# Kernel optimization log

Hardware: AMD Instinct MI355X
Metric: run time of the kernel (lower is better)

The kernel has to match this reference:

```python
import jax, jax.numpy as jnp
import numpy as np

# Constants from UpFIRDn2dJIT(channel=64, lrelu_upsampling=2, filter_size=6, kernel_size=3)
# with init_kernel(in_size=128, out_size=128): up_factor = dn_factor = 2.
UP = 2
DN = 2
SLOPE = 0.2
GAIN = 1.4142135623730951  # sqrt(2)
CROP = 1  # kernel_size - 1 - kernel_size//2 for kernel_size=3
IN_SIZE = 128
FILTER_SIZE = 6
B, C = 8, 64


def _firwin_lowpass(numtaps, cutoff, width, fs):
    # Reproduces scipy.signal.firwin(numtaps, cutoff, width=width, fs=fs)
    # (lowpass, pass_zero=True, scale=True, Kaiser window from `width`).
    nyq = 0.5 * fs
    atten = 2.285 * (numtaps - 1) * np.pi * (width / nyq) + 7.95  # kaiser_atten
    if atten > 50:
        beta = 0.1102 * (atten - 8.7)
    elif atten > 21:
        beta = 0.5842 * (atten - 21) ** 0.4 + 0.07886 * (atten - 21)
    else:
        beta = 0.0
    m = np.arange(numtaps) - (numtaps - 1) / 2.0
    c = cutoff / nyq
    h = c * np.sinc(c * m) * np.kaiser(numtaps, beta)
    h = h / h.sum()  # scale so DC gain == 1
    return h.astype(np.float32)


def _conv1d_same(x, f, axis):
    # x: [N, 1, H, W]; 1D cross-correlation along `axis` (2 or 3) with torch
    # padding='same' semantics for even taps: left pad = (K-1)//2, right pad gets the extra.
    K = f.shape[0]
    pl = (K - 1) // 2
    pr = (K - 1) - pl
    if axis == 2:
        kern = f.reshape(1, 1, K, 1)
        pad = [(pl, pr), (0, 0)]
    else:
        kern = f.reshape(1, 1, 1, K)
        pad = [(0, 0), (pl, pr)]
    return jax.lax.conv_general_dilated(
        x, kern, window_strides=(1, 1), padding=pad,
        dimension_numbers=("NCHW", "OIHW", "NCHW"))


def _forward(x, bias, up_filter, dn_filter):
    x = x[:, :, CROP:-CROP, CROP:-CROP]            # [B, C, 128, 128]
    b, c, h, w = x.shape
    x = x + bias[None, :, None, None]
    x = x.reshape(b * c, 1, h, w)
    x = jnp.repeat(jnp.repeat(x, UP, axis=2), UP, axis=3)
    # outer(f, f) conv == separable 1D convs (filter is an outer product)
    x = _conv1d_same(_conv1d_same(x, up_filter, 2), up_filter, 3)
    x = jnp.where(x >= 0, x, SLOPE * x) * GAIN     # leaky ReLU * gain
    x = _conv1d_same(_conv1d_same(x, dn_filter, 2), dn_filter, 3)
    x = x[:, :, ::DN, ::DN]                        # grid_pool2d -> [B*C, 1, 128, 128]
    return x.reshape(b, c, x.shape[2], x.shape[3])


def setup_inputs() -> dict:
    key = jax.random.key(0)
    kx, = jax.random.split(key, 1)
    x = jax.random.normal(kx, (B, C, IN_SIZE + 2 * CROP, IN_SIZE + 2 * CROP), dtype=jnp.float32)
    bias = jnp.zeros((C,), dtype=jnp.float32)  # nn.Parameter init to zeros
    taps = FILTER_SIZE * UP  # 12
    up_filter = jnp.asarray(_firwin_lowpass(taps, IN_SIZE / 2.0001, IN_SIZE, IN_SIZE))
    dn_filter = jnp.asarray(_firwin_lowpass(taps, IN_SIZE / 2.0001, IN_SIZE, IN_SIZE))
    return {"x": x, "bias": bias, "up_filter": up_filter, "dn_filter": dn_filter}


def reference(x, bias, up_filter, dn_filter):
    return _forward(x, bias, up_filter, dn_filter)
```

## Files before the change

kernel.cpp:

```cpp
#include <hip/hip_runtime.h>


#define GAIN_C 1.4142135623730951f
#define NEG_C ((0.2f - 1.0f) * GAIN_C)

typedef short v8s __attribute__((ext_vector_type(8)));
typedef float v4f __attribute__((ext_vector_type(4)));

__device__ __forceinline__ int f2bf(float f) {
    unsigned u = __float_as_uint(f);
    return (int)((u + 0x7FFFu + ((u >> 16) & 1u)) >> 16) & 0xFFFF;
}
__device__ __forceinline__ int pack_bf2(float a, float b) {
#if __has_builtin(__builtin_amdgcn_cvt_pk_bf16_f32)
    typedef __bf16 bf2 __attribute__((ext_vector_type(2)));
    bf2 r = __builtin_amdgcn_cvt_pk_bf16_f32(a, b);
    int o; __builtin_memcpy(&o, &r, 4); return o;
#else
    return f2bf(a) | (f2bf(b) << 16);
#endif
}

__device__ float band(int x, int q, const float* fu) {
    if (q >= 74 || x >= 43 || x < 0) return 0.f;
    int p = q >> 1, d = x - p;
    if (q & 1) {
        if (d < 0 || d > 6) return 0.f;
        if (d == 0) return fu[0];
        if (d == 6) return fu[11];
        return fu[2 * d - 1] + fu[2 * d];
    } else {
        if (d < 0 || d > 5) return 0.f;
        return fu[2 * d] + fu[2 * d + 1];
    }
}
__device__ float dband(int o, int q, int v, const float* fd) {
    if (q >= 74 || q < 0) return 0.f;
    if (v == 0 && q < 5) return 0.f;
    if (v == 2 && q >= 69) return 0.f;
    int k = q - 2 * o;
    if (k < 0 || k > 11) return 0.f;
    return fd[k];
}

__global__ __launch_bounds__(256) void build_consts(
    const float* __restrict__ fu, const float* __restrict__ fd,
    short* __restrict__ ws)
{
    int idx = blockIdx.x * 256 + threadIdx.x;
    int l = (idx >> 3) & 63, j = idx & 7;
    int l15 = l & 15, kq = (l >> 4) * 8 + j;
    float val;
    if (idx < 2560) {
        int nt = idx >> 9;
        int k0 = 8 * nt < 16 ? 8 * nt : 16;
        val = band(k0 + kq, 16 * nt + l15, fu);
    } else if (idx < 5120) {
        int mt = (idx - 2560) >> 9;
        int k0 = 8 * mt < 16 ? 8 * mt : 16;
        val = band(k0 + kq, 16 * mt + l15, fu);
    } else if (idx < 11264) {
        int rel = idx - 5120;
        int v = rel >> 11, fi = (rel & 2047) >> 9;
        int mt = fi >> 1, kt = fi & 1;
        int pp = (mt ? 16 : 0) + 32 * kt + kq;
        val = dband(16 * mt + l15, pp, v, fd);
    } else {
        int rel = idx - 11264;
        int v = rel >> 11, fi = (rel & 2047) >> 9;
        int nt = fi >> 1, kt = fi & 1;
        int qq = (nt ? 16 : 0) + 32 * kt + kq;
        val = dband(16 * nt + l15, qq, v, fd);
    }
    ws[idx] = (short)f2bf(val);
}

#define XPITCH 48
#define BPITCH 48
#define UPITCH 88
#define TPITCH 80

__global__ __launch_bounds__(320, 8) void upfirdn_mfma(
    const float* __restrict__ xin_all,
    const float* __restrict__ bias,
    const short* __restrict__ cws,
    float* __restrict__ out)
{
    __shared__ __align__(16) short SH[2304 + 3840 + 7040];
    short* Xl  = SH;
    short* B1t = SH + 2304;
    short* Ut  = SH + 6144;
    short* T   = SH;

    const int tid  = threadIdx.x;
    const int lane = tid & 63, w = tid >> 6;
    const int l15  = lane & 15, q4 = lane >> 4;
    const int bx = blockIdx.x, by = blockIdx.y, bc = blockIdx.z;
    const int i0 = by * 32, j0 = bx * 32;

    const short* GtB = cws;
    const short* G2A = cws + 2560;
    const short* DA  = cws + 5120  + ((by == 0) ? 0 : (by == 3) ? 2 : 1) * 2048;
    const short* D2B = cws + 11264 + ((bx == 0) ? 0 : (bx == 3) ? 2 : 1) * 2048;

    {
        const float* xp = xin_all + (size_t)bc * (130 * 130);
        const float bv = bias[bc & 63];
        const bool colInt = (bx == 1) | (bx == 2);
        int* Xli = (int*)Xl;
        for (int idx = tid; idx < 1152; idx += 320) {
            int r = idx / 24, cp = idx - r * 24;
            int gr = i0 - 5 + r;
            float f0 = 0.f, f1 = 0.f;
            if (r < 43 && (unsigned)gr < 128u && cp < 22) {
                const float* rowp = xp + (gr + 1) * 130 + 1;
                int gc0 = j0 - 5 + 2 * cp;
                if (colInt) {
                    f0 = rowp[gc0] + bv;
                    if (cp < 21) f1 = rowp[gc0 + 1] + bv;
                } else {
                    if ((unsigned)gc0 < 128u) f0 = rowp[gc0] + bv;
                    if (cp < 21 && (unsigned)(gc0 + 1) < 128u)
                        f1 = rowp[gc0 + 1] + bv;
                }
            }
            Xli[r * 24 + cp] = pack_bf2(f0, f1);
        }
    }
    __syncthreads();

    {
        const int nt = w;
        const int k0 = 8 * nt < 16 ? 8 * nt : 16;
        v8s bf = *(const v8s*)&GtB[nt * 512 + lane * 8];
#pragma unroll
        for (int mt = 0; mt < 3; ++mt) {
            v8s a = *(const v8s*)&Xl[(16 * mt + l15) * XPITCH + k0 + q4 * 8];
            v4f acc = {0.f, 0.f, 0.f, 0.f};
            acc = __builtin_amdgcn_mfma_f32_16x16x32_bf16(a, bf, acc, 0, 0, 0);
            *(int2*)&B1t[(16 * nt + l15) * BPITCH + 16 * mt + q4 * 4] =
                make_int2(pack_bf2(acc[0], acc[1]), pack_bf2(acc[2], acc[3]));
        }
    }
    __syncthreads();

    {
        const int mt = w;
        const int k0 = 8 * mt < 16 ? 8 * mt : 16;
        v8s af = *(const v8s*)&G2A[mt * 512 + lane * 8];
#pragma unroll
        for (int nt = 0; nt < 5; ++nt) {
            v8s b = *(const v8s*)&B1t[(16 * nt + l15) * BPITCH + k0 + q4 * 8];
            v4f acc = {0.f, 0.f, 0.f, 0.f};
            acc = __builtin_amdgcn_mfma_f32_16x16x32_bf16(af, b, acc, 0, 0, 0);
#pragma unroll
            for (int i = 0; i < 4; ++i)
                acc[i] = GAIN_C * acc[i] + NEG_C * fminf(acc[i], 0.f);
            *(int2*)&Ut[(16 * nt + l15) * UPITCH + 16 * mt + q4 * 4] =
                make_int2(pack_bf2(acc[0], acc[1]), pack_bf2(acc[2], acc[3]));
        }
    }
    __syncthreads();

    {
        const int nt = w;
#pragma unroll
        for (int mt = 0; mt < 2; ++mt) {
            const int k0 = mt ? 16 : 0;
            v4f acc = {0.f, 0.f, 0.f, 0.f};
#pragma unroll
            for (int kt = 0; kt < 2; ++kt) {
                v8s a = *(const v8s*)&DA[(mt * 2 + kt) * 512 + lane * 8];
                v8s b = *(const v8s*)&Ut[(16 * nt + l15) * UPITCH
                                         + k0 + 32 * kt + q4 * 8];
                acc = __builtin_amdgcn_mfma_f32_16x16x32_bf16(a, b, acc, 0, 0, 0);
            }
#pragma unroll
            for (int i = 0; i < 4; ++i)
                T[(16 * mt + q4 * 4 + i) * TPITCH + 16 * nt + l15] =
                    (short)f2bf(acc[i]);
        }
    }
    __syncthreads();

    if (w < 4) {
        const int mt = w >> 1, nt = w & 1;
        const int k0 = nt ? 16 : 0;
        v4f acc = {0.f, 0.f, 0.f, 0.f};
#pragma unroll
        for (int kt = 0; kt < 2; ++kt) {
            v8s a = *(const v8s*)&T[(16 * mt + l15) * TPITCH + k0 + 32 * kt + q4 * 8];
            v8s b = *(const v8s*)&D2B[(nt * 2 + kt) * 512 + lane * 8];
            acc = __builtin_amdgcn_mfma_f32_16x16x32_bf16(a, b, acc, 0, 0, 0);
        }
        float* op = out + (size_t)bc * 16384
                  + (size_t)(i0 + 16 * mt + q4 * 4) * 128 + (j0 + 16 * nt + l15);
#pragma unroll
        for (int i = 0; i < 4; ++i) op[i * 128] = acc[i];
    }
}

extern "C" void kernel_launch(void* const* d_in, const int* in_sizes, int n_in,
                              void* d_out, int out_size, void* d_ws, size_t ws_size,
                              hipStream_t stream) {
    const float* x  = (const float*)d_in[0];
    const float* bs = (const float*)d_in[1];
    const float* fu = (const float*)d_in[2];
    const float* fd = (const float*)d_in[3];
    float* outp = (float*)d_out;
    short* ws = (short*)d_ws;

    build_consts<<<68, 256, 0, stream>>>(fu, fd, ws);
    upfirdn_mfma<<<dim3(4, 4, 512), 320, 0, stream>>>(x, bs, ws, outp);
}
```

Measured before the change: 124.1 us.

## Process two channel planes per block and reorder separable conv passes

Each block now handles two (batch, channel) planes, halving the grid, and loads the constant filter matrices into registers once per block for reuse across both planes. The column and row pass order is swapped, so the transposed scalar writes of the intermediate are replaced by packed int2 stores, and interior row tiles skip bounds checks and use float2 loads. This amortizes constant loads and sync overhead per plane, but doubles shared memory per block and lowers the occupancy hint from 8 to 4 blocks.

```diff
diff --git a/kernel.cpp b/kernel.cpp
--- a/kernel.cpp
+++ b/kernel.cpp
@@ -75,128 +75,142 @@
     ws[idx] = (short)f2bf(val);
 }
 
-#define XPITCH 48
-#define BPITCH 48
-#define UPITCH 88
-#define TPITCH 80
-
-__global__ __launch_bounds__(320, 8) void upfirdn_mfma(
+#define XP2 48
+#define BP2 48
+#define UP2 88
+#define RSZ 13184
+
+__global__ __launch_bounds__(320, 4) void upfirdn_mfma(
     const float* __restrict__ xin_all,
     const float* __restrict__ bias,
     const short* __restrict__ cws,
     float* __restrict__ out)
 {
-    __shared__ __align__(16) short SH[2304 + 3840 + 7040];
-    short* Xl  = SH;
-    short* B1t = SH + 2304;
-    short* Ut  = SH + 6144;
-    short* T   = SH;
+    __shared__ __align__(16) short SH[2 * RSZ];
 
     const int tid  = threadIdx.x;
     const int lane = tid & 63, w = tid >> 6;
     const int l15  = lane & 15, q4 = lane >> 4;
-    const int bx = blockIdx.x, by = blockIdx.y, bc = blockIdx.z;
+    const int bx = blockIdx.x, by = blockIdx.y;
+    const int bc0 = blockIdx.z * 2;
     const int i0 = by * 32, j0 = bx * 32;
 
-    const short* GtB = cws;
-    const short* G2A = cws + 2560;
-    const short* DA  = cws + 5120  + ((by == 0) ? 0 : (by == 3) ? 2 : 1) * 2048;
-    const short* D2B = cws + 11264 + ((bx == 0) ? 0 : (bx == 3) ? 2 : 1) * 2048;
+    const short* DAv  = cws + 5120  + ((by == 0) ? 0 : (by == 3) ? 2 : 1) * 2048;
+    const short* D2Bv = cws + 11264 + ((bx == 0) ? 0 : (bx == 3) ? 2 : 1) * 2048;
+    v8s gtb = *(const v8s*)&cws[w * 512 + lane * 8];
+    v8s g2a = *(const v8s*)&cws[2560 + w * 512 + lane * 8];
+    v8s d2b[4];
+#pragma unroll
+    for (int f = 0; f < 4; ++f) d2b[f] = *(const v8s*)&D2Bv[f * 512 + lane * 8];
+    const int mt4 = (w >> 1) & 1;
+    v8s da0 = *(const v8s*)&DAv[(mt4 * 2 + 0) * 512 + lane * 8];
+    v8s da1 = *(const v8s*)&DAv[(mt4 * 2 + 1) * 512 + lane * 8];
 
     {
-        const float* xp = xin_all + (size_t)bc * (130 * 130);
-        const float bv = bias[bc & 63];
+        const float* xp0 = xin_all + (size_t)bc0 * 16900;
+        const float* xp1 = xp0 + 16900;
+        const float bv0 = bias[bc0 & 63], bv1 = bias[(bc0 + 1) & 63];
+        const bool rowInt = (by == 1) | (by == 2);
         const bool colInt = (bx == 1) | (bx == 2);
-        int* Xli = (int*)Xl;
-        for (int idx = tid; idx < 1152; idx += 320) {
-            int r = idx / 24, cp = idx - r * 24;
+        int* Xli = (int*)SH;
+        for (int idx = tid; idx < 2304; idx += 320) {
+            int pl = (idx >= 1152);
+            int ii = idx - (pl ? 1152 : 0);
+            int r = ii / 24, cp = ii - r * 24;
             int gr = i0 - 5 + r;
+            const float* xp = pl ? xp1 : xp0;
+            const float bv = pl ? bv1 : bv0;
             float f0 = 0.f, f1 = 0.f;
-            if (r < 43 && (unsigned)gr < 128u && cp < 22) {
+            bool rok = (r < 43) && (rowInt || (unsigned)gr < 128u);
+            if (rok && cp < 22) {
+                int gc0 = j0 - 5 + 2 * cp;
                 const float* rowp = xp + (gr + 1) * 130 + 1;
-                int gc0 = j0 - 5 + 2 * cp;
                 if (colInt) {
-                    f0 = rowp[gc0] + bv;
-                    if (cp < 21) f1 = rowp[gc0 + 1] + bv;
+                    float2 v = *(const float2*)(rowp + gc0);
+                    f0 = v.x + bv;
+                    f1 = (cp < 21) ? v.y + bv : 0.f;
                 } else {
                     if ((unsigned)gc0 < 128u) f0 = rowp[gc0] + bv;
                     if (cp < 21 && (unsigned)(gc0 + 1) < 128u)
                         f1 = rowp[gc0 + 1] + bv;
                 }
             }
-            Xli[r * 24 + cp] = pack_bf2(f0, f1);
-        }
-    }
-    __syncthreads();
-
-    {
-        const int nt = w;
-        const int k0 = 8 * nt < 16 ? 8 * nt : 16;
-        v8s bf = *(const v8s*)&GtB[nt * 512 + lane * 8];
+            Xli[pl * (RSZ / 2) + r * 24 + cp] = pack_bf2(f0, f1);
+        }
+    }
+    __syncthreads();
+
+    const int k0u = (8 * w < 16) ? 8 * w : 16;
+
+#pragma unroll
+    for (int pl = 0; pl < 2; ++pl) {
+        const short* Xl  = SH + pl * RSZ;
+        short*       B1t = SH + pl * RSZ + 2304;
 #pragma unroll
         for (int mt = 0; mt < 3; ++mt) {
-            v8s a = *(const v8s*)&Xl[(16 * mt + l15) * XPITCH + k0 + q4 * 8];
-            v4f acc = {0.f, 0.f, 0.f, 0.f};
-            acc = __builtin_amdgcn_mfma_f32_16x16x32_bf16(a, bf, acc, 0, 0, 0);
-            *(int2*)&B1t[(16 * nt + l15) * BPITCH + 16 * mt + q4 * 4] =
+            v8s a = *(const v8s*)&Xl[(16 * mt + l15) * XP2 + k0u + q4 * 8];
+            v4f acc = {0.f, 0.f, 0.f, 0.f};
+            acc = __builtin_amdgcn_mfma_f32_16x16x32_bf16(a, gtb, acc, 0, 0, 0);
+            *(int2*)&B1t[(16 * w + l15) * BP2 + 16 * mt + q4 * 4] =
                 make_int2(pack_bf2(acc[0], acc[1]), pack_bf2(acc[2], acc[3]));
         }
     }
     __syncthreads();
 
-    {
-        const int mt = w;
-        const int k0 = 8 * mt < 16 ? 8 * mt : 16;
-        v8s af = *(const v8s*)&G2A[mt * 512 + lane * 8];
-#pragma unroll
-        for (int nt = 0; nt < 5; ++nt) {
-            v8s b = *(const v8s*)&B1t[(16 * nt + l15) * BPITCH + k0 + q4 * 8];
-            v4f acc = {0.f, 0.f, 0.f, 0.f};
-            acc = __builtin_amdgcn_mfma_f32_16x16x32_bf16(af, b, acc, 0, 0, 0);
+#pragma unroll
+    for (int pl = 0; pl < 2; ++pl) {
+        const short* B1t = SH + pl * RSZ + 2304;
+        short*       U   = SH + pl * RSZ + 6144;
+#pragma unroll
+        for (int mt = 0; mt < 5; ++mt) {
+            v8s a = *(const v8s*)&B1t[(16 * mt + l15) * BP2 + k0u + q4 * 8];
+            v4f acc = {0.f, 0.f, 0.f, 0.f};
+            acc = __builtin_amdgcn_mfma_f32_16x16x32_bf16(a, g2a, acc, 0, 0, 0);
 #pragma unroll
             for (int i = 0; i < 4; ++i)
                 acc[i] = GAIN_C * acc[i] + NEG_C * fminf(acc[i], 0.f);
-            *(int2*)&Ut[(16 * nt + l15) * UPITCH + 16 * mt + q4 * 4] =
+            *(int2*)&U[(16 * w + l15) * UP2 + 16 * mt + q4 * 4] =
                 make_int2(pack_bf2(acc[0], acc[1]), pack_bf2(acc[2], acc[3]));
         }
     }
     __syncthreads();
 
-    {
-        const int nt = w;
-#pragma unroll
-        for (int mt = 0; mt < 2; ++mt) {
-            const int k0 = mt ? 16 : 0;
+#pragma unroll
+    for (int pl = 0; pl < 2; ++pl) {
+        const short* U = SH + pl * RSZ + 6144;
+        short*       V = SH + pl * RSZ;
+#pragma unroll
+        for (int nt = 0; nt < 2; ++nt) {
+            const int k0 = nt ? 16 : 0;
             v4f acc = {0.f, 0.f, 0.f, 0.f};
 #pragma unroll
             for (int kt = 0; kt < 2; ++kt) {
-                v8s a = *(const v8s*)&DA[(mt * 2 + kt) * 512 + lane * 8];
-                v8s b = *(const v8s*)&Ut[(16 * nt + l15) * UPITCH
-                                         + k0 + 32 * kt + q4 * 8];
-                acc = __builtin_amdgcn_mfma_f32_16x16x32_bf16(a, b, acc, 0, 0, 0);
+                v8s a = *(const v8s*)&U[(16 * w + l15) * UP2 + k0 + 32 * kt + q4 * 8];
+                acc = __builtin_amdgcn_mfma_f32_16x16x32_bf16(a, d2b[nt * 2 + kt],
+                                                              acc, 0, 0, 0);
             }
-#pragma unroll
-            for (int i = 0; i < 4; ++i)
-                T[(16 * mt + q4 * 4 + i) * TPITCH + 16 * nt + l15] =
-                    (short)f2bf(acc[i]);
+            *(int2*)&V[(16 * nt + l15) * UP2 + 16 * w + q4 * 4] =
+                make_int2(pack_bf2(acc[0], acc[1]), pack_bf2(acc[2], acc[3]));
         }
     }
     __syncthreads();
 
     if (w < 4) {
         const int mt = w >> 1, nt = w & 1;
-        const int k0 = nt ? 16 : 0;
-        v4f acc = {0.f, 0.f, 0.f, 0.f};
-#pragma unroll
-        for (int kt = 0; kt < 2; ++kt) {
-            v8s a = *(const v8s*)&T[(16 * mt + l15) * TPITCH + k0 + 32 * kt + q4 * 8];
-            v8s b = *(const v8s*)&D2B[(nt * 2 + kt) * 512 + lane * 8];
-            acc = __builtin_amdgcn_mfma_f32_16x16x32_bf16(a, b, acc, 0, 0, 0);
-        }
-        float* op = out + (size_t)bc * 16384
-                  + (size_t)(i0 + 16 * mt + q4 * 4) * 128 + (j0 + 16 * nt + l15);
-#pragma unroll
-        for (int i = 0; i < 4; ++i) op[i * 128] = acc[i];
+        const int k0 = mt ? 16 : 0;
+#pragma unroll
+        for (int pl = 0; pl < 2; ++pl) {
+            const short* V = SH + pl * RSZ;
+            v4f acc = {0.f, 0.f, 0.f, 0.f};
+            v8s b0 = *(const v8s*)&V[(16 * nt + l15) * UP2 + k0 + q4 * 8];
+            v8s b1 = *(const v8s*)&V[(16 * nt + l15) * UP2 + k0 + 32 + q4 * 8];
+            acc = __builtin_amdgcn_mfma_f32_16x16x32_bf16(da0, b0, acc, 0, 0, 0);
+            acc = __builtin_amdgcn_mfma_f32_16x16x32_bf16(da1, b1, acc, 0, 0, 0);
+            float* op = out + (size_t)(bc0 + pl) * 16384
+                      + (size_t)(i0 + 16 * mt + q4 * 4) * 128 + (j0 + 16 * nt + l15);
+#pragma unroll
+            for (int i = 0; i < 4; ++i) op[i * 128] = acc[i];
+        }
     }
 }
 
@@ -211,5 +225,5 @@
     short* ws = (short*)d_ws;
 
     build_consts<<<68, 256, 0, stream>>>(fu, fd, ws);
-    upfirdn_mfma<<<dim3(4, 4, 512), 320, 0, stream>>>(x, bs, ws, outp);
-}
+    upfirdn_mfma<<<dim3(4, 4, 256), 320, 0, stream>>>(x, bs, ws, outp);
+}
```

Result: slower. 162.8 us (+31.2%).
